# Kernel tuning notes

Measured on AMD Instinct MI355X. Metric: run time of the kernel, lower is better.

## Reference

```python
import jax, jax.numpy as jnp
import numpy as np

D_MODEL = 1024
H = 16
D_K = D_MODEL // H
NEG = -1e9


def setup_inputs() -> dict:
    key = jax.random.key(0)
    ks = jax.random.split(key, 12)
    B, S = 4, 2048
    scale = 1.0 / np.sqrt(D_MODEL)
    return {
        "q": jax.random.normal(ks[0], (B, S, D_MODEL), dtype=jnp.float32),
        "k": jax.random.normal(ks[1], (B, S, D_MODEL), dtype=jnp.float32),
        "v": jax.random.normal(ks[2], (B, S, D_MODEL), dtype=jnp.float32),
        "mask": jnp.ones((1, 1, S, S), dtype=jnp.int32),
        "w_q": jax.random.normal(ks[3], (D_MODEL, D_MODEL), dtype=jnp.float32) * scale,
        "b_q": jnp.zeros((D_MODEL,), dtype=jnp.float32),
        "w_k": jax.random.normal(ks[4], (D_MODEL, D_MODEL), dtype=jnp.float32) * scale,
        "b_k": jnp.zeros((D_MODEL,), dtype=jnp.float32),
        "w_v": jax.random.normal(ks[5], (D_MODEL, D_MODEL), dtype=jnp.float32) * scale,
        "b_v": jnp.zeros((D_MODEL,), dtype=jnp.float32),
        "w_o": jax.random.normal(ks[6], (D_MODEL, D_MODEL), dtype=jnp.float32) * scale,
        "b_o": jnp.zeros((D_MODEL,), dtype=jnp.float32),
    }


def reference(q, k, v, mask, w_q, b_q, w_k, b_k, w_v, b_v, w_o, b_o):
    B, S, _ = q.shape
    # projections (torch Linear: x @ W^T + b)
    query = q @ w_q.T + b_q
    key = k @ w_k.T + b_k
    value = v @ w_v.T + b_v
    # [B, S, D] -> [B, H, S, d_k]
    query = query.reshape(B, S, H, D_K).transpose(0, 2, 1, 3)
    key = key.reshape(B, S, H, D_K).transpose(0, 2, 1, 3)
    value = value.reshape(B, S, H, D_K).transpose(0, 2, 1, 3)
    # scaled dot-product attention, full [B,H,S,S] scores as in original
    scores = jnp.einsum("bhqd,bhkd->bhqk", query, key) / jnp.sqrt(
        jnp.asarray(D_K, dtype=query.dtype)
    )
    scores = jnp.where(mask == 0, jnp.asarray(NEG, dtype=scores.dtype), scores)
    attn = jax.nn.softmax(scores, axis=-1)
    x = jnp.einsum("bhqk,bhkd->bhqd", attn, value)
    # [B, H, S, d_k] -> [B, S, D]
    x = x.transpose(0, 2, 1, 3).reshape(B, S, H * D_K)
    return x @ w_o.T + b_o
```

## Files before the change

### kernel.cpp

```cpp
#include <hip/hip_runtime.h>

typedef unsigned short u16;
typedef unsigned int u32;
typedef unsigned long long u64;
typedef __attribute__((ext_vector_type(8))) short short8;
typedef __attribute__((ext_vector_type(4))) float f32x4;
typedef __attribute__((ext_vector_type(16))) float f32x16;
typedef __attribute__((ext_vector_type(4))) u32 u32x4;

constexpr int S_LEN = 2048;
constexpr int DMODEL = 1024;

#if __has_builtin(__builtin_amdgcn_exp2f)
#define EXP2 __builtin_amdgcn_exp2f
#else
#define EXP2 exp2f
#endif

__device__ __forceinline__ u16 f2bf(float f) {
  u32 u = __builtin_bit_cast(u32, f);
  u += 0x7FFFu + ((u >> 16) & 1u);
  return (u16)(u >> 16);
}

__device__ __forceinline__ u32 cvtpk(float a, float b) {
  u32 r;
  asm("v_cvt_pk_bf16_f32 %0, %1, %2" : "=v"(r) : "v"(a), "v"(b));
  return r;
}

__device__ __forceinline__ void plswap(u32& a, u32& b) {
  asm("v_permlane32_swap_b32 %0, %1" : "+v"(a), "+v"(b));
}

__device__ __forceinline__ void gload_lds16(const void* g, void* l) {
  __builtin_amdgcn_global_load_lds((const __attribute__((address_space(1))) u32*)g,
                                   (__attribute__((address_space(3))) u32*)l,
                                   16, 0, 0);
}

__global__ __launch_bounds__(256) void cvt_w_kernel(
    const float* __restrict__ w0, const float* __restrict__ w1,
    const float* __restrict__ w2, const float* __restrict__ w3,
    u16* __restrict__ o0, u16* __restrict__ o1,
    u16* __restrict__ o2, u16* __restrict__ o3) {
  const float* src; u16* dst;
  switch (blockIdx.y) {
    case 0: src = w0; dst = o0; break;
    case 1: src = w1; dst = o1; break;
    case 2: src = w2; dst = o2; break;
    default: src = w3; dst = o3; break;
  }
  int i = blockIdx.x * 256 + threadIdx.x;
  float4 v = ((const float4*)src)[i];
  ushort4 h;
  h.x = f2bf(v.x); h.y = f2bf(v.y); h.z = f2bf(v.z); h.w = f2bf(v.w);
  ((ushort4*)dst)[i] = h;
}

__global__ __launch_bounds__(256) void cvt_a_kernel(
    const float* __restrict__ src, u16* __restrict__ dst) {
  int i = blockIdx.x * 256 + threadIdx.x;
  float4 v = ((const float4*)src)[i];
  ushort4 h;
  h.x = f2bf(v.x); h.y = f2bf(v.y); h.z = f2bf(v.z); h.w = f2bf(v.w);
  ((ushort4*)dst)[i] = h;
}

__global__ __launch_bounds__(256) void mask_pack_kernel(
    const int* __restrict__ mask, u64* __restrict__ mb) {
  int gw = (blockIdx.x * 256 + threadIdx.x) >> 6;
  int lane = threadIdx.x & 63;
  #pragma unroll
  for (int i = 0; i < 16; ++i) {
    size_t word = (size_t)gw * 16 + i;
    int m = mask[word * 64 + lane];
    u64 bits = __ballot(m != 0);
    if (lane == 0) mb[word] = bits;
  }
}

template<int OM>
__global__ __launch_bounds__(256) void gemm_bt_kernel(
    const u16* __restrict__ A, const u16* __restrict__ W,
    const float* __restrict__ bias, void* __restrict__ Cv, float scale) {
  constexpr int BK = 32;
  __shared__ __align__(16) u16 As[128 * BK];
  __shared__ __align__(16) u16 Bs[128 * BK];
  const int tid = threadIdx.x;
  const int lane = tid & 63, w = tid >> 6;
  const int l15 = lane & 15, lg = lane >> 4;
  const int m0 = blockIdx.x * 128, n0 = blockIdx.y * 128;
  const int wm = w >> 1, wn = w & 1;
  f32x4 acc[4][4] = {};

  for (int kt = 0; kt < 1024; kt += BK) {
    #pragma unroll
    for (int j = 0; j < 2; ++j) {
      int sb = (w * 2 + j) * 64;
      int slot = sb + lane;
      int row = slot >> 2, c8 = slot & 3;
      gload_lds16(W + (size_t)(n0 + row) * 1024 + kt + c8 * 8,
                  (char*)Bs + (size_t)sb * 16);
      gload_lds16(A + (size_t)(m0 + row) * 1024 + kt + c8 * 8,
                  (char*)As + (size_t)sb * 16);
    }
    __syncthreads();
    short8 af[4], bfr[4];
    #pragma unroll
    for (int m = 0; m < 4; ++m)
      af[m] = *(const short8*)&As[(wm * 64 + m * 16 + l15) * BK + lg * 8];
    #pragma unroll
    for (int n = 0; n < 4; ++n)
      bfr[n] = *(const short8*)&Bs[(wn * 64 + n * 16 + l15) * BK + lg * 8];
    #pragma unroll
    for (int m = 0; m < 4; ++m)
      #pragma unroll
      for (int n = 0; n < 4; ++n)
        acc[m][n] = __builtin_amdgcn_mfma_f32_16x16x32_bf16(af[m], bfr[n], acc[m][n], 0, 0, 0);
    __syncthreads();
  }

  #pragma unroll
  for (int m = 0; m < 4; ++m) {
    #pragma unroll
    for (int n = 0; n < 4; ++n) {
      int col = n0 + wn * 64 + n * 16 + l15;
      float bcol = bias[col];
      int row0 = m0 + wm * 64 + m * 16 + lg * 4;
      if constexpr (OM == 2) {
        int b = row0 >> 11, s = row0 & 2047;
        ushort4 o;
        o.x = f2bf((acc[m][n][0] + bcol) * scale);
        o.y = f2bf((acc[m][n][1] + bcol) * scale);
        o.z = f2bf((acc[m][n][2] + bcol) * scale);
        o.w = f2bf((acc[m][n][3] + bcol) * scale);
        u16* dst = (u16*)Cv + ((size_t)(b * 16 + (col >> 6)) * 64 + (col & 63)) * S_LEN + s;
        *(ushort4*)dst = o;
      } else {
        #pragma unroll
        for (int r = 0; r < 4; ++r) {
          float v = (acc[m][n][r] + bcol) * scale;
          if constexpr (OM == 1)
            ((float*)Cv)[(size_t)(row0 + r) * 1024 + col] = v;
          else
            ((u16*)Cv)[(size_t)(row0 + r) * 1024 + col] = f2bf(v);
        }
      }
    }
  }
}

__global__ __launch_bounds__(256, 4) void attn_kernel(
    const u16* __restrict__ Qp, const u16* __restrict__ Kp,
    const u16* __restrict__ VpT, const u64* __restrict__ mb,
    u16* __restrict__ X) {
  constexpr float NEGL2 = -1.4426950e9f;
  __shared__ __align__(16) u16 Ks[2][4096];
  __shared__ __align__(16) u16 VTs[2][4096];
  const int tid = threadIdx.x;
  const int lane = tid & 63, w = tid >> 6;
  const int l31 = lane & 31, hi1 = lane >> 5;

  u32 id = blockIdx.x;
  u32 nid = ((id & 7) << 7) | (id >> 3);
  const int bh = nid >> 4, qt = nid & 15;
  const int b = bh >> 4, h = bh & 15;
  const size_t bS = (size_t)b * S_LEN;
  const int wq0 = qt * 128 + w * 32;

  short8 qf[4];
  {
    const u16* qb = Qp + (bS + wq0 + l31) * DMODEL + h * 64;
    #pragma unroll
    for (int dk = 0; dk < 4; ++dk)
      qf[dk] = *(const short8*)(qb + dk * 16 + hi1 * 8);
  }

  f32x16 xacc[2] = {};
  float lsum = 0.f;

  auto stage = [&](int k0, int nb) {
    #pragma unroll
    for (int i = 0; i < 2; ++i) {
      int g = tid + i * 256;
      int kk = g >> 3, dh = g & 7;
      gload_lds16(Kp + (bS + k0 + kk) * DMODEL + h * 64 + ((dh ^ (kk & 7)) << 3),
                  (char*)&Ks[nb][0] + g * 16);
    }
    #pragma unroll
    for (int i = 0; i < 2; ++i) {
      int g = tid + i * 256;
      int dd = g >> 3, kh = g & 7;
      gload_lds16(VpT + ((size_t)(bh * 64 + dd)) * S_LEN + k0 + ((kh ^ (dd & 7)) << 3),
                  (char*)&VTs[nb][0] + g * 16);
    }
  };

  stage(0, 0);
  __syncthreads();

  constexpr int NT = S_LEN / 64;
  for (int t = 0; t < NT; ++t) {
    const int cur = t & 1;
    if (t + 1 < NT) stage((t + 1) * 64, cur ^ 1);

    f32x16 c0, c1;
    #pragma unroll
    for (int r = 0; r < 16; ++r) { c0[r] = -16.f; c1[r] = -16.f; }
    const u16* ksp = &Ks[cur][0];
    __builtin_amdgcn_s_setprio(1);
    #pragma unroll
    for (int dk = 0; dk < 4; ++dk) {
      short8 a0 = *(const short8*)&ksp[((l31) * 64 + dk * 16 + hi1 * 8) ^ ((l31 & 7) << 3)];
      short8 a1 = *(const short8*)&ksp[((32 + l31) * 64 + dk * 16 + hi1 * 8) ^ ((l31 & 7) << 3)];
      c0 = __builtin_amdgcn_mfma_f32_32x32x16_bf16(a0, qf[dk], c0, 0, 0, 0);
      c1 = __builtin_amdgcn_mfma_f32_32x32x16_bf16(a1, qf[dk], c1, 0, 0, 0);
    }
    __builtin_amdgcn_s_setprio(0);

    u64 mw = mb[(size_t)(wq0 + l31) * 32 + t];
    bool allone = __all((long long)mw == -1LL);
    if (!allone) {
      #pragma unroll
      for (int r = 0; r < 16; ++r) {
        int k0i = (r & 3) + 8 * (r >> 2) + 4 * hi1;
        c0[r] = ((mw >> k0i) & 1) ? c0[r] : NEGL2;
        c1[r] = ((mw >> (k0i + 32)) & 1) ? c1[r] : NEGL2;
      }
    }

    float ls = 0.f;
    #pragma unroll
    for (int r = 0; r < 16; ++r) { float p = EXP2(c0[r]); c0[r] = p; ls += p; }
    #pragma unroll
    for (int r = 0; r < 16; ++r) { float p = EXP2(c1[r]); c1[r] = p; ls += p; }
    lsum += ls;

    u32 Wp[2][8];
    #pragma unroll
    for (int i = 0; i < 8; ++i) {
      Wp[0][i] = cvtpk(c0[2 * i], c0[2 * i + 1]);
      Wp[1][i] = cvtpk(c1[2 * i], c1[2 * i + 1]);
    }

    const u16* vtp = &VTs[cur][0];
    __builtin_amdgcn_s_setprio(1);
    #pragma unroll
    for (int ks16 = 0; ks16 < 4; ++ks16) {
      const int kc = ks16 >> 1, ks = ks16 & 1;
      u32 wa0 = Wp[kc][ks * 4 + 0], wb0 = Wp[kc][ks * 4 + 2];
      u32 wa1 = Wp[kc][ks * 4 + 1], wb1 = Wp[kc][ks * 4 + 3];
      plswap(wa0, wb0);
      plswap(wa1, wb1);
      u32x4 pw; pw.x = wa0; pw.y = wa1; pw.z = wb0; pw.w = wb1;
      short8 pfrag = __builtin_bit_cast(short8, pw);
      #pragma unroll
      for (int dt = 0; dt < 2; ++dt) {
        int d = dt * 32 + l31;
        short8 vf = *(const short8*)&vtp[(d * 64 + ks16 * 16 + hi1 * 8) ^ ((d & 7) << 3)];
        xacc[dt] = __builtin_amdgcn_mfma_f32_32x32x16_bf16(vf, pfrag, xacc[dt], 0, 0, 0);
      }
    }
    __builtin_amdgcn_s_setprio(0);
    __syncthreads();
  }

  lsum += __shfl_xor(lsum, 32);
  float inv = 1.0f / lsum;
  u16* xb = X + (bS + wq0 + l31) * DMODEL + h * 64;
  #pragma unroll
  for (int dt = 0; dt < 2; ++dt)
    #pragma unroll
    for (int m = 0; m < 4; ++m) {
      ushort4 o;
      o.x = f2bf(xacc[dt][m * 4 + 0] * inv);
      o.y = f2bf(xacc[dt][m * 4 + 1] * inv);
      o.z = f2bf(xacc[dt][m * 4 + 2] * inv);
      o.w = f2bf(xacc[dt][m * 4 + 3] * inv);
      *(ushort4*)(xb + dt * 32 + m * 8 + hi1 * 4) = o;
    }
}

extern "C" void kernel_launch(void* const* d_in, const int* in_sizes, int n_in,
                              void* d_out, int out_size, void* d_ws, size_t ws_size,
                              hipStream_t stream) {
  const float* q  = (const float*)d_in[0];
  const float* k  = (const float*)d_in[1];
  const float* v  = (const float*)d_in[2];
  const int* mask = (const int*)d_in[3];
  const float* wq = (const float*)d_in[4];
  const float* bq = (const float*)d_in[5];
  const float* wk = (const float*)d_in[6];
  const float* bk = (const float*)d_in[7];
  const float* wv = (const float*)d_in[8];
  const float* bv = (const float*)d_in[9];
  const float* wo = (const float*)d_in[10];
  const float* bo = (const float*)d_in[11];

  char* ws = (char*)d_ws;
  u16* wqb = (u16*)(ws + 0x000000);
  u16* wkb = (u16*)(ws + 0x200000);
  u16* wvb = (u16*)(ws + 0x400000);
  u16* wob = (u16*)(ws + 0x600000);
  u64* mbp = (u64*)(ws + 0x800000);
  u16* Qp  = (u16*)(ws + 0x880000);
  u16* Kp  = (u16*)(ws + 0x1880000);
  u16* Xp  = (u16*)(ws + 0x3880000);
  u16* VpT = (u16*)(ws + 0x4880000);

  const float QSCALE = 0.125f * 1.44269504088896340736f;
  u16* Ab = Xp;

  cvt_w_kernel<<<dim3(1024, 4), 256, 0, stream>>>(wq, wk, wv, wo, wqb, wkb, wvb, wob);
  mask_pack_kernel<<<1024, 256, 0, stream>>>(mask, mbp);

  cvt_a_kernel<<<8192, 256, 0, stream>>>(v, Ab);
  gemm_bt_kernel<2><<<dim3(64, 8), 256, 0, stream>>>(Ab, wvb, bv, VpT, 1.0f);

  cvt_a_kernel<<<8192, 256, 0, stream>>>(k, Ab);
  gemm_bt_kernel<0><<<dim3(64, 8), 256, 0, stream>>>(Ab, wkb, bk, Kp, 1.0f);

  cvt_a_kernel<<<8192, 256, 0, stream>>>(q, Ab);
  gemm_bt_kernel<0><<<dim3(64, 8), 256, 0, stream>>>(Ab, wqb, bq, Qp, QSCALE);

  attn_kernel<<<1024, 256, 0, stream>>>(Qp, Kp, VpT, mbp, Xp);
  gemm_bt_kernel<1><<<dim3(64, 8), 256, 0, stream>>>(Xp, wob, bo, (float*)d_out, 1.0f);
}
```

Measured before the change: 245.1 us.

## Double-buffer GEMM LDS tiles, split PV accumulators, merge prep kernels

```diff
diff --git a/kernel.cpp b/kernel.cpp
--- a/kernel.cpp
+++ b/kernel.cpp
@@ -39,11 +39,24 @@
                                    16, 0, 0);
 }
 
-__global__ __launch_bounds__(256) void cvt_w_kernel(
+__global__ __launch_bounds__(256) void prep_kernel(
     const float* __restrict__ w0, const float* __restrict__ w1,
     const float* __restrict__ w2, const float* __restrict__ w3,
     u16* __restrict__ o0, u16* __restrict__ o1,
-    u16* __restrict__ o2, u16* __restrict__ o3) {
+    u16* __restrict__ o2, u16* __restrict__ o3,
+    const int* __restrict__ mask, u64* __restrict__ mb) {
+  if (blockIdx.y == 4) {
+    int gw = (blockIdx.x * 256 + threadIdx.x) >> 6;
+    int lane = threadIdx.x & 63;
+    #pragma unroll
+    for (int i = 0; i < 16; ++i) {
+      size_t word = (size_t)gw * 16 + i;
+      int m = mask[word * 64 + lane];
+      u64 bits = __ballot(m != 0);
+      if (lane == 0) mb[word] = bits;
+    }
+    return;
+  }
   const float* src; u16* dst;
   switch (blockIdx.y) {
     case 0: src = w0; dst = o0; break;
@@ -67,26 +80,13 @@
   ((ushort4*)dst)[i] = h;
 }
 
-__global__ __launch_bounds__(256) void mask_pack_kernel(
-    const int* __restrict__ mask, u64* __restrict__ mb) {
-  int gw = (blockIdx.x * 256 + threadIdx.x) >> 6;
-  int lane = threadIdx.x & 63;
-  #pragma unroll
-  for (int i = 0; i < 16; ++i) {
-    size_t word = (size_t)gw * 16 + i;
-    int m = mask[word * 64 + lane];
-    u64 bits = __ballot(m != 0);
-    if (lane == 0) mb[word] = bits;
-  }
-}
-
 template<int OM>
 __global__ __launch_bounds__(256) void gemm_bt_kernel(
     const u16* __restrict__ A, const u16* __restrict__ W,
     const float* __restrict__ bias, void* __restrict__ Cv, float scale) {
   constexpr int BK = 32;
-  __shared__ __align__(16) u16 As[128 * BK];
-  __shared__ __align__(16) u16 Bs[128 * BK];
+  __shared__ __align__(16) u16 As[2][128 * BK];
+  __shared__ __align__(16) u16 Bs[2][128 * BK];
   const int tid = threadIdx.x;
   const int lane = tid & 63, w = tid >> 6;
   const int l15 = lane & 15, lg = lane >> 4;
@@ -94,25 +94,33 @@
   const int wm = w >> 1, wn = w & 1;
   f32x4 acc[4][4] = {};
 
-  for (int kt = 0; kt < 1024; kt += BK) {
+  auto stage = [&](int kt, int nb) {
     #pragma unroll
     for (int j = 0; j < 2; ++j) {
       int sb = (w * 2 + j) * 64;
       int slot = sb + lane;
       int row = slot >> 2, c8 = slot & 3;
       gload_lds16(W + (size_t)(n0 + row) * 1024 + kt + c8 * 8,
-                  (char*)Bs + (size_t)sb * 16);
+                  (char*)&Bs[nb][0] + (size_t)sb * 16);
       gload_lds16(A + (size_t)(m0 + row) * 1024 + kt + c8 * 8,
-                  (char*)As + (size_t)sb * 16);
-    }
-    __syncthreads();
+                  (char*)&As[nb][0] + (size_t)sb * 16);
+    }
+  };
+
+  stage(0, 0);
+  __syncthreads();
+
+  constexpr int NK = 1024 / BK;
+  for (int ki = 0; ki < NK; ++ki) {
+    const int cur = ki & 1;
+    if (ki + 1 < NK) stage((ki + 1) * BK, cur ^ 1);
     short8 af[4], bfr[4];
     #pragma unroll
     for (int m = 0; m < 4; ++m)
-      af[m] = *(const short8*)&As[(wm * 64 + m * 16 + l15) * BK + lg * 8];
+      af[m] = *(const short8*)&As[cur][(wm * 64 + m * 16 + l15) * BK + lg * 8];
     #pragma unroll
     for (int n = 0; n < 4; ++n)
-      bfr[n] = *(const short8*)&Bs[(wn * 64 + n * 16 + l15) * BK + lg * 8];
+      bfr[n] = *(const short8*)&Bs[cur][(wn * 64 + n * 16 + l15) * BK + lg * 8];
     #pragma unroll
     for (int m = 0; m < 4; ++m)
       #pragma unroll
@@ -177,7 +185,7 @@
       qf[dk] = *(const short8*)(qb + dk * 16 + hi1 * 8);
   }
 
-  f32x16 xacc[2] = {};
+  f32x16 xaccE[2] = {}, xaccO[2] = {};
   float lsum = 0.f;
 
   auto stage = [&](int k0, int nb) {
@@ -255,11 +263,12 @@
       plswap(wa1, wb1);
       u32x4 pw; pw.x = wa0; pw.y = wa1; pw.z = wb0; pw.w = wb1;
       short8 pfrag = __builtin_bit_cast(short8, pw);
+      f32x16* xt = (ks16 & 1) ? xaccO : xaccE;
       #pragma unroll
       for (int dt = 0; dt < 2; ++dt) {
         int d = dt * 32 + l31;
         short8 vf = *(const short8*)&vtp[(d * 64 + ks16 * 16 + hi1 * 8) ^ ((d & 7) << 3)];
-        xacc[dt] = __builtin_amdgcn_mfma_f32_32x32x16_bf16(vf, pfrag, xacc[dt], 0, 0, 0);
+        xt[dt] = __builtin_amdgcn_mfma_f32_32x32x16_bf16(vf, pfrag, xt[dt], 0, 0, 0);
       }
     }
     __builtin_amdgcn_s_setprio(0);
@@ -274,10 +283,10 @@
     #pragma unroll
     for (int m = 0; m < 4; ++m) {
       ushort4 o;
-      o.x = f2bf(xacc[dt][m * 4 + 0] * inv);
-      o.y = f2bf(xacc[dt][m * 4 + 1] * inv);
-      o.z = f2bf(xacc[dt][m * 4 + 2] * inv);
-      o.w = f2bf(xacc[dt][m * 4 + 3] * inv);
+      o.x = f2bf((xaccE[dt][m * 4 + 0] + xaccO[dt][m * 4 + 0]) * inv);
+      o.y = f2bf((xaccE[dt][m * 4 + 1] + xaccO[dt][m * 4 + 1]) * inv);
+      o.z = f2bf((xaccE[dt][m * 4 + 2] + xaccO[dt][m * 4 + 2]) * inv);
+      o.w = f2bf((xaccE[dt][m * 4 + 3] + xaccO[dt][m * 4 + 3]) * inv);
       *(ushort4*)(xb + dt * 32 + m * 8 + hi1 * 4) = o;
     }
 }
@@ -312,8 +321,8 @@
   const float QSCALE = 0.125f * 1.44269504088896340736f;
   u16* Ab = Xp;
 
-  cvt_w_kernel<<<dim3(1024, 4), 256, 0, stream>>>(wq, wk, wv, wo, wqb, wkb, wvb, wob);
-  mask_pack_kernel<<<1024, 256, 0, stream>>>(mask, mbp);
+  prep_kernel<<<dim3(1024, 5), 256, 0, stream>>>(wq, wk, wv, wo, wqb, wkb, wvb, wob,
+                                                 mask, mbp);
 
   cvt_a_kernel<<<8192, 256, 0, stream>>>(v, Ab);
   gemm_bt_kernel<2><<<dim3(64, 8), 256, 0, stream>>>(Ab, wvb, bv, VpT, 1.0f);
```

New measurement: 355.4 us. 1.45x slower.
